# Performance work log

Hardware: AMD Instinct MI355X
Metric: run time of the kernel (lower is better)

The kernel has to match this reference:

```python
import jax, jax.numpy as jnp
import numpy as np

# Module hyperparameters (init_kwargs): dim=128, res=128, idx=0, split_size=8, num_heads=8
B, RES, DIM, NH = 8, 128, 128, 8
HD = DIM // NH               # head_dim = 16
HSP, WSP = RES, 8            # idx=0 -> H_sp=res, W_sp=split_size
N = HSP * WSP                # tokens per window
SCALE = HD ** -0.5
L = RES * RES


def setup_inputs() -> dict:
    key = jax.random.key(0)
    k1, k2, k3 = jax.random.split(key, 3)
    return {
        "qkv": jax.random.normal(k1, (3, B, L, DIM), dtype=jnp.float32),
        "conv_w": jax.random.normal(k2, (DIM, 1, 3, 3), dtype=jnp.float32) * 0.1,
        "conv_b": jax.random.normal(k3, (DIM,), dtype=jnp.float32) * 0.1,
    }


def _im2cswin(x):
    # x: [B, L, C] -> windows as heads: [B*nW, NH, N, HD]
    x = jnp.transpose(x, (0, 2, 1)).reshape(B, DIM, RES, RES)
    x = x.reshape(B, DIM, RES // HSP, HSP, RES // WSP, WSP)
    x = jnp.transpose(x, (0, 2, 4, 3, 5, 1)).reshape(-1, N, DIM)
    x = x.reshape(-1, N, NH, HD)
    return jnp.transpose(x, (0, 2, 1, 3))


def reference(qkv, conv_w, conv_b):
    q, k, v = qkv[0], qkv[1], qkv[2]
    k = _im2cswin(k)                               # [W, NH, N, HD]
    v = _im2cswin(v)                               # [W, NH, N, HD]

    # q -> per-window image blocks [B*nW, C, H_sp, W_sp]
    qi = jnp.transpose(q, (0, 2, 1)).reshape(B, DIM, RES, RES)
    qi = qi.reshape(B, DIM, RES // HSP, HSP, RES // WSP, WSP)
    qi = jnp.transpose(qi, (0, 2, 4, 1, 3, 5)).reshape(-1, DIM, HSP, WSP)

    # depthwise 3x3 conv LePE
    lepe = jax.lax.conv_general_dilated(
        qi, conv_w, window_strides=(1, 1), padding='SAME',
        feature_group_count=DIM,
        dimension_numbers=('NCHW', 'OIHW', 'NCHW'))
    lepe = lepe + conv_b[None, :, None, None]
    lepe = jnp.transpose(lepe.reshape(-1, NH, HD, N), (0, 1, 3, 2))  # [W, NH, N, HD]
    qh = jnp.transpose(qi.reshape(-1, NH, HD, N), (0, 1, 3, 2))      # [W, NH, N, HD]

    # linear attention: softmax over scaled K^T V (d x d)
    att = jnp.einsum('wnid,wnie->wnde', k, v) * SCALE                # [W, NH, HD, HD]
    att = jax.nn.softmax(att, axis=-1)
    x = jnp.einsum('wnid,wnde->wnie', qh, att) + lepe                # [W, NH, N, HD]

    # windows -> image -> [B, L, C]
    x = jnp.transpose(x, (0, 2, 1, 3)).reshape(-1, N, DIM)
    x = x.reshape(B, RES // HSP, RES // WSP, HSP, WSP, DIM)
    x = jnp.transpose(x, (0, 1, 3, 2, 4, 5)).reshape(B, RES, RES, DIM)
    return x.reshape(B, L, DIM)
```

## Files before the change

### kernel.cpp

```cpp
#include <hip/hip_runtime.h>


static constexpr int BB   = 8;
static constexpr int RES  = 128;
static constexpr int DIM  = 128;
static constexpr int WSP  = 8;
static constexpr int L    = RES * RES;
static constexpr float SCALE = 0.25f;

#define GLD_LDS16(g, l)                                                        \
  __builtin_amdgcn_global_load_lds(                                            \
      (const __attribute__((address_space(1))) void*)(const void*)(g),         \
      (__attribute__((address_space(3))) void*)(l), 16, 0, 0)

__global__ __launch_bounds__(256, 2) void fused_lepe(
    const float* __restrict__ Qg, const float* __restrict__ Kg,
    const float* __restrict__ Vg, const float* __restrict__ cw,
    const float* __restrict__ cb, float* __restrict__ outp) {
  __shared__ float smem[12288];
  float* const A_sm    = smem + 9216;
  float* const scratch = smem + 10240;

  const int b  = blockIdx.x;
  const int w  = b >> 2, g = b & 3;
  const int bi = w >> 4, wb = w & 15;
  const int t  = threadIdx.x;
  const int wave = t >> 6, lane = t & 63;
  const size_t win_base = (size_t)(bi * L + wb * WSP) * DIM;
  const int ch0 = g * 32;

  const int combo = lane & 15;
  const int split = lane >> 4;
  const int h1 = combo >> 3, dgrp = (combo >> 2) & 1, eq = combo & 3;
  const int koff = h1 * 16 + dgrp * 8;
  const int voff = h1 * 16 + eq * 4;
  const int n0 = (wave * 4 + split) * 4;

  float4 acc[8];
#pragma unroll
  for (int i = 0; i < 8; ++i) acc[i] = make_float4(0.f, 0.f, 0.f, 0.f);

  auto stageKV = [&](int tile, int buf) {
    for (int c = wave; c < 16; c += 4) {
      const int mat = c >> 3, rr = c & 7;
      const float* src = (mat ? Vg : Kg) + win_base +
                         (size_t)(tile * 8 + rr) * (RES * DIM) +
                         (lane >> 3) * DIM + ch0 + (lane & 7) * 4;
      float* dst = smem + mat * 6144 + buf * 2048 + rr * 256;
      GLD_LDS16(src, dst);
    }
  };

  stageKV(0, 0);
  stageKV(1, 1);
  for (int tt = 0; tt < 16; ++tt) {
    if (tt < 15) asm volatile("s_waitcnt vmcnt(4)" ::: "memory");
    else         asm volatile("s_waitcnt vmcnt(0)" ::: "memory");
    __builtin_amdgcn_s_barrier();
    if (tt + 2 < 16) stageKV(tt + 2, (tt + 2) % 3);
    const float* Kb = smem + (tt % 3) * 2048;
    const float* Vb = smem + 6144 + (tt % 3) * 2048;
#pragma unroll
    for (int i = 0; i < 4; ++i) {
      const int n = n0 + i;
      const float4 k0 = *reinterpret_cast<const float4*>(&Kb[n * 32 + koff]);
      const float4 k1 = *reinterpret_cast<const float4*>(&Kb[n * 32 + koff + 4]);
      const float4 v  = *reinterpret_cast<const float4*>(&Vb[n * 32 + voff]);
#define FMA4(a, s)                                                             \
  a.x += (s) * v.x; a.y += (s) * v.y; a.z += (s) * v.z; a.w += (s) * v.w;
      FMA4(acc[0], k0.x) FMA4(acc[1], k0.y) FMA4(acc[2], k0.z) FMA4(acc[3], k0.w)
      FMA4(acc[4], k1.x) FMA4(acc[5], k1.y) FMA4(acc[6], k1.z) FMA4(acc[7], k1.w)
#undef FMA4
    }
  }

#pragma unroll
  for (int i = 0; i < 8; ++i) {
    acc[i].x += __shfl_xor(acc[i].x, 16); acc[i].y += __shfl_xor(acc[i].y, 16);
    acc[i].z += __shfl_xor(acc[i].z, 16); acc[i].w += __shfl_xor(acc[i].w, 16);
    acc[i].x += __shfl_xor(acc[i].x, 32); acc[i].y += __shfl_xor(acc[i].y, 32);
    acc[i].z += __shfl_xor(acc[i].z, 32); acc[i].w += __shfl_xor(acc[i].w, 32);
  }
  if (lane < 16) {
    float* sc = scratch + wave * 512 + combo * 32;
#pragma unroll
    for (int i = 0; i < 8; ++i)
      *reinterpret_cast<float4*>(&sc[i * 4]) = acc[i];
  }
  __syncthreads();

  auto stageQ = [&](int tile, int buf) {
    const int r0 = tile * 16;
    float* qb = smem + buf * 4608;
    for (int c = wave; c < 18; c += 4) {
      const int r = r0 - 1 + c;
      float* dst = qb + c * 256;
      if ((unsigned)r < 128u) {
        const float* src = Qg + win_base + (size_t)r * (RES * DIM) +
                           (lane >> 3) * DIM + ch0 +
                           (((lane & 7) ^ (c & 7)) << 2);
        GLD_LDS16(src, dst);
      } else {
        *reinterpret_cast<float4*>(dst + lane * 4) =
            make_float4(0.f, 0.f, 0.f, 0.f);
      }
    }
  };
  stageQ(0, 0);

  {
    const int r = t >> 3, e2 = t & 7;
    const int cmb = (r >> 4) * 8 + ((r >> 3) & 1) * 4 + (e2 >> 1);
    const float* s0 = scratch + cmb * 32 + (r & 7) * 4 + (e2 & 1) * 2;
    float v0 = (s0[0] + s0[512] + s0[1024] + s0[1536]) * SCALE;
    float v1 = (s0[1] + s0[513] + s0[1025] + s0[1537]) * SCALE;
    float m = fmaxf(v0, v1);
    m = fmaxf(m, __shfl_xor(m, 1));
    m = fmaxf(m, __shfl_xor(m, 2));
    m = fmaxf(m, __shfl_xor(m, 4));
    v0 = __expf(v0 - m); v1 = __expf(v1 - m);
    float ss = v0 + v1;
    ss += __shfl_xor(ss, 1);
    ss += __shfl_xor(ss, 2);
    ss += __shfl_xor(ss, 4);
    const float ri = 1.0f / ss;
    A_sm[r * 16 + e2 * 2 + 0] = v0 * ri;
    A_sm[r * 16 + e2 * 2 + 1] = v1 * ri;
  }
  __syncthreads();

  const int cq   = t & 7;
  const int lr   = (t >> 3) & 15;
  const int half = t >> 7;
  const int hg = cq >> 2, e0 = (cq & 3) * 4;
  const int cg = ch0 + cq * 4;

  float4 Acol[16];
#pragma unroll
  for (int d = 0; d < 16; ++d)
    Acol[d] = *reinterpret_cast<const float4*>(&A_sm[(hg * 16 + d) * 16 + e0]);
  float4 wgt[9];
#pragma unroll
  for (int tap = 0; tap < 9; ++tap) {
    wgt[tap].x = cw[(cg + 0) * 9 + tap];
    wgt[tap].y = cw[(cg + 1) * 9 + tap];
    wgt[tap].z = cw[(cg + 2) * 9 + tap];
    wgt[tap].w = cw[(cg + 3) * 9 + tap];
  }
  const float4 bias = *reinterpret_cast<const float4*>(&cb[cg]);
  const float4 zero4 = make_float4(0.f, 0.f, 0.f, 0.f);

#define ACC(qs, d)                                                             \
  o.x += (qs) * Acol[d].x; o.y += (qs) * Acol[d].y;                            \
  o.z += (qs) * Acol[d].z; o.w += (qs) * Acol[d].w;

  int buf = 0;
  for (int tile = 0; tile < 8; ++tile) {
    if (tile < 7) stageQ(tile + 1, buf ^ 1);
    const float* Qb = smem + buf * 4608;
    const int r0 = tile * 16;
    const int w0 = half * 4;

    float4 cL[3], cC[3], cR[3];
    auto ldcol = [&](int cidx, float4* dv) {
#pragma unroll
      for (int dy = 0; dy < 3; ++dy) {
        const int br = lr + dy;
        dv[dy] = ((unsigned)cidx < 8u)
                     ? *reinterpret_cast<const float4*>(
                           &Qb[(br * 8 + cidx) * 32 + ((cq ^ (br & 7)) << 2)])
                     : zero4;
      }
    };
    ldcol(w0 - 1, cL);
    ldcol(w0, cC);

#pragma unroll
    for (int k = 0; k < 4; ++k) {
      const int wl = w0 + k;
      ldcol(wl + 1, cR);
      float4 o = bias;
#pragma unroll
      for (int dy = 0; dy < 3; ++dy) {
        const int t0 = dy * 3;
        o.x += cL[dy].x * wgt[t0].x + cC[dy].x * wgt[t0+1].x + cR[dy].x * wgt[t0+2].x;
        o.y += cL[dy].y * wgt[t0].y + cC[dy].y * wgt[t0+1].y + cR[dy].y * wgt[t0+2].y;
        o.z += cL[dy].z * wgt[t0].z + cC[dy].z * wgt[t0+1].z + cR[dy].z * wgt[t0+2].z;
        o.w += cL[dy].w * wgt[t0].w + cC[dy].w * wgt[t0+1].w + cR[dy].w * wgt[t0+2].w;
      }
      {
        const int br1 = lr + 1, sw = br1 & 7;
        const float* qb0 = &Qb[(br1 * 8 + wl) * 32];
        const float4 q0 = *reinterpret_cast<const float4*>(qb0 + (((hg*4+0)^sw)<<2));
        const float4 q1 = *reinterpret_cast<const float4*>(qb0 + (((hg*4+1)^sw)<<2));
        const float4 q2 = *reinterpret_cast<const float4*>(qb0 + (((hg*4+2)^sw)<<2));
        const float4 q3 = *reinterpret_cast<const float4*>(qb0 + (((hg*4+3)^sw)<<2));
        ACC(q0.x, 0)  ACC(q0.y, 1)  ACC(q0.z, 2)  ACC(q0.w, 3)
        ACC(q1.x, 4)  ACC(q1.y, 5)  ACC(q1.z, 6)  ACC(q1.w, 7)
        ACC(q2.x, 8)  ACC(q2.y, 9)  ACC(q2.z, 10) ACC(q2.w, 11)
        ACC(q3.x, 12) ACC(q3.y, 13) ACC(q3.z, 14) ACC(q3.w, 15)
      }
      float* dst = outp + win_base + (size_t)(r0 + lr) * (RES * DIM) +
                   wl * DIM + cg;
      *reinterpret_cast<float4*>(dst) = o;

#pragma unroll
      for (int dy = 0; dy < 3; ++dy) { cL[dy] = cC[dy]; cC[dy] = cR[dy]; }
    }
    __syncthreads();
    buf ^= 1;
  }
#undef ACC
}

extern "C" void kernel_launch(void* const* d_in, const int* in_sizes, int n_in,
                              void* d_out, int out_size, void* d_ws,
                              size_t ws_size, hipStream_t stream) {
  const float* qkv = (const float*)d_in[0];
  const float* cw  = (const float*)d_in[1];
  const float* cb  = (const float*)d_in[2];
  const float* Qg = qkv;
  const float* Kg = qkv + (size_t)BB * L * DIM;
  const float* Vg = Kg + (size_t)BB * L * DIM;
  float* outp = (float*)d_out;

  fused_lepe<<<512, 256, 0, stream>>>(Qg, Kg, Vg, cw, cb, outp);
}
```

Measured before the change: 67.51 us.

## Use double-buffered 16-row KV tiles and drop Q LDS swizzle

Restructures the K/V reduction from a triple-buffered pipeline of 8-row tiles with fine-grained vmcnt waits into a double-buffered pipeline of 16-row tiles synchronised with __syncthreads. Each thread now handles 8 tokens per tile. Shared memory is regrouped so the reduction scratch aliases the start of the buffer, and the first Q tile is prefetched before the scratch write. The XOR swizzle on Q staging and reads is removed to simplify addressing. The cost is a larger LDS footprint, coarser overlap of loads with compute, and possible LDS bank conflicts on Q reads.

```diff
diff --git a/kernel.cpp b/kernel.cpp
--- a/kernel.cpp
+++ b/kernel.cpp
@@ -17,9 +17,9 @@
     const float* __restrict__ Qg, const float* __restrict__ Kg,
     const float* __restrict__ Vg, const float* __restrict__ cw,
     const float* __restrict__ cb, float* __restrict__ outp) {
-  __shared__ float smem[12288];
-  float* const A_sm    = smem + 9216;
-  float* const scratch = smem + 10240;
+  __shared__ float smem[16896];
+  float* const A_sm    = smem + 16384;
+  float* const scratch = smem;
 
   const int b  = blockIdx.x;
   const int w  = b >> 2, g = b & 3;
@@ -34,34 +34,33 @@
   const int h1 = combo >> 3, dgrp = (combo >> 2) & 1, eq = combo & 3;
   const int koff = h1 * 16 + dgrp * 8;
   const int voff = h1 * 16 + eq * 4;
-  const int n0 = (wave * 4 + split) * 4;
+  const int n0 = (wave * 4 + split) * 8;
 
   float4 acc[8];
 #pragma unroll
   for (int i = 0; i < 8; ++i) acc[i] = make_float4(0.f, 0.f, 0.f, 0.f);
 
   auto stageKV = [&](int tile, int buf) {
-    for (int c = wave; c < 16; c += 4) {
-      const int mat = c >> 3, rr = c & 7;
+    for (int c = wave; c < 32; c += 4) {
+      const int mat = c >> 4, rr = c & 15;
+      const int r = tile * 16 + rr;
       const float* src = (mat ? Vg : Kg) + win_base +
-                         (size_t)(tile * 8 + rr) * (RES * DIM) +
-                         (lane >> 3) * DIM + ch0 + (lane & 7) * 4;
-      float* dst = smem + mat * 6144 + buf * 2048 + rr * 256;
+                         (size_t)r * (RES * DIM) + (lane >> 3) * DIM + ch0 +
+                         (lane & 7) * 4;
+      float* dst = smem + mat * 8192 + buf * 4096 + rr * 256;
       GLD_LDS16(src, dst);
     }
   };
 
   stageKV(0, 0);
-  stageKV(1, 1);
-  for (int tt = 0; tt < 16; ++tt) {
-    if (tt < 15) asm volatile("s_waitcnt vmcnt(4)" ::: "memory");
-    else         asm volatile("s_waitcnt vmcnt(0)" ::: "memory");
-    __builtin_amdgcn_s_barrier();
-    if (tt + 2 < 16) stageKV(tt + 2, (tt + 2) % 3);
-    const float* Kb = smem + (tt % 3) * 2048;
-    const float* Vb = smem + 6144 + (tt % 3) * 2048;
-#pragma unroll
-    for (int i = 0; i < 4; ++i) {
+  __syncthreads();
+  for (int tt = 0; tt < 8; ++tt) {
+    const int cur = tt & 1;
+    if (tt < 7) stageKV(tt + 1, cur ^ 1);
+    const float* Kb = smem + cur * 4096;
+    const float* Vb = smem + 8192 + cur * 4096;
+#pragma unroll 2
+    for (int i = 0; i < 8; ++i) {
       const int n = n0 + i;
       const float4 k0 = *reinterpret_cast<const float4*>(&Kb[n * 32 + koff]);
       const float4 k1 = *reinterpret_cast<const float4*>(&Kb[n * 32 + koff + 4]);
@@ -72,6 +71,7 @@
       FMA4(acc[4], k1.x) FMA4(acc[5], k1.y) FMA4(acc[6], k1.z) FMA4(acc[7], k1.w)
 #undef FMA4
     }
+    __syncthreads();
   }
 
 #pragma unroll
@@ -81,13 +81,6 @@
     acc[i].x += __shfl_xor(acc[i].x, 32); acc[i].y += __shfl_xor(acc[i].y, 32);
     acc[i].z += __shfl_xor(acc[i].z, 32); acc[i].w += __shfl_xor(acc[i].w, 32);
   }
-  if (lane < 16) {
-    float* sc = scratch + wave * 512 + combo * 32;
-#pragma unroll
-    for (int i = 0; i < 8; ++i)
-      *reinterpret_cast<float4*>(&sc[i * 4]) = acc[i];
-  }
-  __syncthreads();
 
   auto stageQ = [&](int tile, int buf) {
     const int r0 = tile * 16;
@@ -97,8 +90,7 @@
       float* dst = qb + c * 256;
       if ((unsigned)r < 128u) {
         const float* src = Qg + win_base + (size_t)r * (RES * DIM) +
-                           (lane >> 3) * DIM + ch0 +
-                           (((lane & 7) ^ (c & 7)) << 2);
+                           (lane >> 3) * DIM + ch0 + (lane & 7) * 4;
         GLD_LDS16(src, dst);
       } else {
         *reinterpret_cast<float4*>(dst + lane * 4) =
@@ -106,7 +98,15 @@
       }
     }
   };
-  stageQ(0, 0);
+
+  stageQ(0, 1);
+  if (lane < 16) {
+    float* sc = scratch + wave * 512 + combo * 32;
+#pragma unroll
+    for (int i = 0; i < 8; ++i)
+      *reinterpret_cast<float4*>(&sc[i * 4]) = acc[i];
+  }
+  __syncthreads();
 
   {
     const int r = t >> 3, e2 = t & 7;
@@ -154,7 +154,7 @@
   o.x += (qs) * Acol[d].x; o.y += (qs) * Acol[d].y;                            \
   o.z += (qs) * Acol[d].z; o.w += (qs) * Acol[d].w;
 
-  int buf = 0;
+  int buf = 1;
   for (int tile = 0; tile < 8; ++tile) {
     if (tile < 7) stageQ(tile + 1, buf ^ 1);
     const float* Qb = smem + buf * 4608;
@@ -164,13 +164,11 @@
     float4 cL[3], cC[3], cR[3];
     auto ldcol = [&](int cidx, float4* dv) {
 #pragma unroll
-      for (int dy = 0; dy < 3; ++dy) {
-        const int br = lr + dy;
+      for (int dy = 0; dy < 3; ++dy)
         dv[dy] = ((unsigned)cidx < 8u)
                      ? *reinterpret_cast<const float4*>(
-                           &Qb[(br * 8 + cidx) * 32 + ((cq ^ (br & 7)) << 2)])
+                           &Qb[((lr + dy) * 8 + cidx) * 32 + cq * 4])
                      : zero4;
-      }
     };
     ldcol(w0 - 1, cL);
     ldcol(w0, cC);
@@ -188,18 +186,16 @@
         o.z += cL[dy].z * wgt[t0].z + cC[dy].z * wgt[t0+1].z + cR[dy].z * wgt[t0+2].z;
         o.w += cL[dy].w * wgt[t0].w + cC[dy].w * wgt[t0+1].w + cR[dy].w * wgt[t0+2].w;
       }
-      {
-        const int br1 = lr + 1, sw = br1 & 7;
-        const float* qb0 = &Qb[(br1 * 8 + wl) * 32];
-        const float4 q0 = *reinterpret_cast<const float4*>(qb0 + (((hg*4+0)^sw)<<2));
-        const float4 q1 = *reinterpret_cast<const float4*>(qb0 + (((hg*4+1)^sw)<<2));
-        const float4 q2 = *reinterpret_cast<const float4*>(qb0 + (((hg*4+2)^sw)<<2));
-        const float4 q3 = *reinterpret_cast<const float4*>(qb0 + (((hg*4+3)^sw)<<2));
-        ACC(q0.x, 0)  ACC(q0.y, 1)  ACC(q0.z, 2)  ACC(q0.w, 3)
-        ACC(q1.x, 4)  ACC(q1.y, 5)  ACC(q1.z, 6)  ACC(q1.w, 7)
-        ACC(q2.x, 8)  ACC(q2.y, 9)  ACC(q2.z, 10) ACC(q2.w, 11)
-        ACC(q3.x, 12) ACC(q3.y, 13) ACC(q3.z, 14) ACC(q3.w, 15)
-      }
+      const float* qr = &Qb[((lr + 1) * 8 + wl) * 32 + hg * 16];
+      const float4 q0 = *reinterpret_cast<const float4*>(qr + 0);
+      const float4 q1 = *reinterpret_cast<const float4*>(qr + 4);
+      const float4 q2 = *reinterpret_cast<const float4*>(qr + 8);
+      const float4 q3 = *reinterpret_cast<const float4*>(qr + 12);
+      ACC(q0.x, 0)  ACC(q0.y, 1)  ACC(q0.z, 2)  ACC(q0.w, 3)
+      ACC(q1.x, 4)  ACC(q1.y, 5)  ACC(q1.z, 6)  ACC(q1.w, 7)
+      ACC(q2.x, 8)  ACC(q2.y, 9)  ACC(q2.z, 10) ACC(q2.w, 11)
+      ACC(q3.x, 12) ACC(q3.y, 13) ACC(q3.z, 14) ACC(q3.w, 15)
+
       float* dst = outp + win_base + (size_t)(r0 + lr) * (RES * DIM) +
                    wl * DIM + cg;
       *reinterpret_cast<float4*>(dst) = o;
```

Result: faster. 59.13 us (median of 2 runs) (-12.4%).
